# Kernel tuning notes

Hardware: AMD Instinct MI355X
Metric: run time of the kernel (lower is better)

Reference implementation:

```python
import jax, jax.numpy as jnp
import numpy as np

EMBD = 16
NUM_NODES = 100000
NUM_EDGES = 3200000
BN_EPS = 1e-5


def setup_inputs() -> dict:
    key = jax.random.key(0)
    ks = jax.random.split(key, 12)
    x = jax.random.normal(ks[0], (NUM_NODES, EMBD), dtype=jnp.float32)
    edge_index = jax.random.randint(ks[1], (2, NUM_EDGES), 0, NUM_NODES, dtype=jnp.int64)
    edge_attr = jax.random.normal(ks[2], (NUM_EDGES, EMBD), dtype=jnp.float32)
    s = 1.0 / np.sqrt(EMBD)  # torch Linear default init scale
    W0 = jax.random.uniform(ks[3], (EMBD, EMBD), jnp.float32, -s, s)
    b0 = jax.random.uniform(ks[4], (EMBD,), jnp.float32, -s, s)
    W1 = jax.random.uniform(ks[5], (EMBD, EMBD), jnp.float32, -s, s)
    b1 = jax.random.uniform(ks[6], (EMBD,), jnp.float32, -s, s)
    W2 = jax.random.uniform(ks[7], (EMBD, EMBD), jnp.float32, -s, s)
    b2 = jax.random.uniform(ks[8], (EMBD,), jnp.float32, -s, s)
    gamma = jnp.ones((EMBD,), jnp.float32)
    beta = jnp.zeros((EMBD,), jnp.float32)
    return {"x": x, "edge_index": edge_index, "edge_attr": edge_attr,
            "W0": W0, "b0": b0, "W1": W1, "b1": b1, "W2": W2, "b2": b2,
            "gamma": gamma, "beta": beta}


def reference(x, edge_index, edge_attr, W0, b0, W1, b1, W2, b2, gamma, beta):
    # Gather source/dest node features per edge: (num_edges, embd)
    h_src = x[edge_index[0]]
    h_dest = x[edge_index[1]]
    # Three small linears (torch Linear: y = x @ W.T + b), summed
    e = (edge_attr @ W0.T + b0) + (h_src @ W1.T + b1) + (h_dest @ W2.T + b2)
    # BatchNorm1d in training mode: biased batch statistics over edge dim
    mean = jnp.mean(e, axis=0)
    var = jnp.var(e, axis=0)  # biased, matches torch normalization
    e = (e - mean) * jax.lax.rsqrt(var + BN_EPS) * gamma + beta
    # ReLU + residual
    return edge_attr + jax.nn.relu(e)
```

## Files before the change

kernel.cpp:

```cpp
#include <hip/hip_runtime.h>
#include <math.h>

#define NN 100000
#define NE 3200000

constexpr int BLK = 256;
constexpr int GRID_EDGE = 2048;

typedef float f4 __attribute__((ext_vector_type(4)));
typedef _Float16 h4 __attribute__((ext_vector_type(4)));
typedef _Float16 h8 __attribute__((ext_vector_type(8)));


__device__ __forceinline__ void matvec16_acc(const float* __restrict__ sW,
                                             const float v[16], float acc[16]) {
#pragma unroll
  for (int j = 0; j < 16; ++j) {
    float a = acc[j];
#pragma unroll
    for (int q = 0; q < 4; ++q) {
      float4 w = ((const float4*)(sW + j * 16))[q];
      a = fmaf(v[q * 4 + 0], w.x, a);
      a = fmaf(v[q * 4 + 1], w.y, a);
      a = fmaf(v[q * 4 + 2], w.z, a);
      a = fmaf(v[q * 4 + 3], w.w, a);
    }
    acc[j] = a;
  }
}

__device__ __forceinline__ void load_row16(const float* __restrict__ base,
                                           size_t row, float v[16]) {
  const f4* r = (const f4*)(base + row * 16);
#pragma unroll
  for (int q = 0; q < 4; ++q) {
    f4 t = r[q];
    v[q * 4 + 0] = t[0]; v[q * 4 + 1] = t[1];
    v[q * 4 + 2] = t[2]; v[q * 4 + 3] = t[3];
  }
}

__device__ __forceinline__ void load_row16_nt(const float* __restrict__ base,
                                              size_t row, float v[16]) {
  const f4* r = (const f4*)(base + row * 16);
#pragma unroll
  for (int q = 0; q < 4; ++q) {
    f4 t = __builtin_nontemporal_load(r + q);
    v[q * 4 + 0] = t[0]; v[q * 4 + 1] = t[1];
    v[q * 4 + 2] = t[2]; v[q * 4 + 3] = t[3];
  }
}

__device__ __forceinline__ h8 pack_h8(const float* v) {
  h8 o;
#pragma unroll
  for (int i = 0; i < 8; ++i) o[i] = (_Float16)v[i];
  return o;
}

__global__ __launch_bounds__(BLK)
void node_proj(const float* __restrict__ x, const float* __restrict__ W1,
               const float* __restrict__ W2, h8* __restrict__ p1h,
               h8* __restrict__ p2h) {
  __shared__ __align__(16) float sW1[256];
  __shared__ __align__(16) float sW2[256];
  for (int i = threadIdx.x; i < 256; i += BLK) { sW1[i] = W1[i]; sW2[i] = W2[i]; }
  __syncthreads();
  int n = blockIdx.x * BLK + threadIdx.x;
  if (n >= NN) return;
  float xv[16];
  load_row16(x, (size_t)n, xv);
  float y1[16], y2[16];
#pragma unroll
  for (int j = 0; j < 16; ++j) { y1[j] = 0.f; y2[j] = 0.f; }
  matvec16_acc(sW1, xv, y1);
  matvec16_acc(sW2, xv, y2);
  p1h[(size_t)n * 2 + 0] = pack_h8(y1);
  p1h[(size_t)n * 2 + 1] = pack_h8(y1 + 8);
  p2h[(size_t)n * 2 + 0] = pack_h8(y2);
  p2h[(size_t)n * 2 + 1] = pack_h8(y2 + 8);
}

template <bool TABS, bool EH>
__global__ __launch_bounds__(BLK)
void edge_pass1(const float* __restrict__ ea, const int* __restrict__ ei,
                const float* __restrict__ xO, const h8* __restrict__ p1h,
                const h8* __restrict__ p2h, const float* __restrict__ W0g,
                const float* __restrict__ W1g, const float* __restrict__ W2g,
                float* __restrict__ stats, _Float16* __restrict__ eh,
                float* __restrict__ out) {
  __shared__ __align__(16) float sW0[256];
  __shared__ __align__(16) float sW1[256];
  __shared__ __align__(16) float sW2[256];
  __shared__ float red[4][32];
  for (int i = threadIdx.x; i < 256; i += BLK) {
    sW0[i] = W0g[i];
    if (!TABS) { sW1[i] = W1g[i]; sW2[i] = W2g[i]; }
  }
  __syncthreads();

  float sum[16], ssq[16];
#pragma unroll
  for (int j = 0; j < 16; ++j) { sum[j] = 0.f; ssq[j] = 0.f; }

  const int total = gridDim.x * BLK;
  for (int e = blockIdx.x * BLK + threadIdx.x; e < NE; e += total) {
    int s = __builtin_nontemporal_load(ei + e);
    int d = __builtin_nontemporal_load(ei + NE + e);
    float eav[16];
    load_row16_nt(ea, (size_t)e, eav);
    float ev[16];
    if (TABS) {
      h8 a0 = p1h[(size_t)s * 2 + 0];
      h8 a1 = p1h[(size_t)s * 2 + 1];
      h8 b0 = p2h[(size_t)d * 2 + 0];
      h8 b1 = p2h[(size_t)d * 2 + 1];
#pragma unroll
      for (int j = 0; j < 8; ++j) {
        ev[j]     = (float)a0[j] + (float)b0[j];
        ev[8 + j] = (float)a1[j] + (float)b1[j];
      }
      matvec16_acc(sW0, eav, ev);
    } else {
      float xs[16], xd[16];
      load_row16(xO, (size_t)s, xs);
      load_row16(xO, (size_t)d, xd);
#pragma unroll
      for (int j = 0; j < 16; ++j) ev[j] = 0.f;
      matvec16_acc(sW0, eav, ev);
      matvec16_acc(sW1, xs, ev);
      matvec16_acc(sW2, xd, ev);
    }
#pragma unroll
    for (int j = 0; j < 16; ++j) {
      sum[j] += ev[j];
      ssq[j] = fmaf(ev[j], ev[j], ssq[j]);
    }
    if (EH) {
      h8* ep = (h8*)(eh + (size_t)e * 16);
      __builtin_nontemporal_store(pack_h8(ev), ep);
      __builtin_nontemporal_store(pack_h8(ev + 8), ep + 1);
    } else {
      f4* orow = (f4*)(out + (size_t)e * 16);
#pragma unroll
      for (int q = 0; q < 4; ++q) {
        f4 o;
        o[0] = ev[q * 4 + 0]; o[1] = ev[q * 4 + 1];
        o[2] = ev[q * 4 + 2]; o[3] = ev[q * 4 + 3];
        __builtin_nontemporal_store(o, orow + q);
      }
    }
  }

#pragma unroll
  for (int off = 32; off > 0; off >>= 1) {
#pragma unroll
    for (int j = 0; j < 16; ++j) {
      sum[j] += __shfl_down(sum[j], off);
      ssq[j] += __shfl_down(ssq[j], off);
    }
  }
  int wid = threadIdx.x >> 6;
  int lane = threadIdx.x & 63;
  if (lane == 0) {
#pragma unroll
    for (int j = 0; j < 16; ++j) {
      red[wid][j] = sum[j];
      red[wid][16 + j] = ssq[j];
    }
  }
  __syncthreads();
  if (threadIdx.x < 32) {
    float v = red[0][threadIdx.x] + red[1][threadIdx.x] +
              red[2][threadIdx.x] + red[3][threadIdx.x];
    atomicAdd(stats + threadIdx.x, v);
  }
}

__global__ void finalize_kernel(const float* __restrict__ stats,
                                const float* __restrict__ gamma,
                                const float* __restrict__ beta,
                                float* __restrict__ ss) {
  int j = threadIdx.x;
  if (j < 16) {
    const float inv_n = 1.0f / (float)NE;
    float mean = stats[j] * inv_n;
    float var = fmaf(-mean, mean, stats[16 + j] * inv_n);
    float sc = gamma[j] / sqrtf(var + 1e-5f);
    ss[j] = sc;
    ss[16 + j] = fmaf(-mean, sc, beta[j]);
  }
}

template <bool EH>
__global__ __launch_bounds__(BLK)
void edge_pass2(const float* __restrict__ ea, const _Float16* __restrict__ eh,
                const float* __restrict__ ssg, float* __restrict__ out) {
  __shared__ float sSS[32];
  if (threadIdx.x < 32) sSS[threadIdx.x] = ssg[threadIdx.x];
  __syncthreads();
  const int totalv = NE * 4;
  const int stride = gridDim.x * BLK;
  int i0 = blockIdx.x * BLK + threadIdx.x;
  int c = (i0 & 3) * 4;
  float sc0 = sSS[c + 0], sc1 = sSS[c + 1], sc2 = sSS[c + 2], sc3 = sSS[c + 3];
  float sh0 = sSS[16 + c + 0], sh1 = sSS[16 + c + 1];
  float sh2 = sSS[16 + c + 2], sh3 = sSS[16 + c + 3];
  for (int i = i0; i < totalv; i += stride) {
    f4 av = __builtin_nontemporal_load((const f4*)ea + i);
    f4 evv;
    if (EH) {
      h4 hv = __builtin_nontemporal_load((const h4*)eh + i);
      evv[0] = (float)hv[0]; evv[1] = (float)hv[1];
      evv[2] = (float)hv[2]; evv[3] = (float)hv[3];
    } else {
      evv = __builtin_nontemporal_load((const f4*)out + i);
    }
    f4 o;
    o[0] = av[0] + fmaxf(0.f, fmaf(evv[0], sc0, sh0));
    o[1] = av[1] + fmaxf(0.f, fmaf(evv[1], sc1, sh1));
    o[2] = av[2] + fmaxf(0.f, fmaf(evv[2], sc2, sh2));
    o[3] = av[3] + fmaxf(0.f, fmaf(evv[3], sc3, sh3));
    __builtin_nontemporal_store(o, (f4*)out + i);
  }
}

extern "C" void kernel_launch(void* const* d_in, const int* in_sizes, int n_in,
                              void* d_out, int out_size, void* d_ws, size_t ws_size,
                              hipStream_t stream) {
  const float* x     = (const float*)d_in[0];
  const int*   ei    = (const int*)d_in[1];
  const float* ea    = (const float*)d_in[2];
  const float* W0    = (const float*)d_in[3];
  const float* W1    = (const float*)d_in[5];
  const float* W2    = (const float*)d_in[7];
  const float* gamma = (const float*)d_in[9];
  const float* beta  = (const float*)d_in[10];
  float* out = (float*)d_out;

  float* ws    = (float*)d_ws;
  float* stats = ws;
  float* ss    = ws + 32;
  h8* p1h = (h8*)((char*)d_ws + 1024);
  h8* p2h = p1h + (size_t)NN * 2;
  _Float16* eh = (_Float16*)(p2h + (size_t)NN * 2);

  size_t need_tabs = 1024 + (size_t)NN * 64;
  size_t need_eh   = need_tabs + (size_t)NE * 32;
  bool has_tabs = ws_size >= need_tabs;
  bool has_eh   = ws_size >= need_eh;

  hipMemsetAsync(stats, 0, 32 * sizeof(float), stream);

  if (has_tabs) {
    node_proj<<<(NN + BLK - 1) / BLK, BLK, 0, stream>>>(x, W1, W2, p1h, p2h);
    if (has_eh)
      edge_pass1<true, true><<<GRID_EDGE, BLK, 0, stream>>>(
          ea, ei, x, p1h, p2h, W0, W1, W2, stats, eh, out);
    else
      edge_pass1<true, false><<<GRID_EDGE, BLK, 0, stream>>>(
          ea, ei, x, p1h, p2h, W0, W1, W2, stats, eh, out);
  } else {
    edge_pass1<false, false><<<GRID_EDGE, BLK, 0, stream>>>(
        ea, ei, x, p1h, p2h, W0, W1, W2, stats, eh, out);
  }

  finalize_kernel<<<1, 64, 0, stream>>>(stats, gamma, beta, ss);

  if (has_eh)
    edge_pass2<true><<<GRID_EDGE, BLK, 0, stream>>>(ea, eh, ss, out);
  else
    edge_pass2<false><<<GRID_EDGE, BLK, 0, stream>>>(ea, eh, ss, out);
}
```

Measured before the change: 578.9 us.

## Fold stats zeroing and BN finalize into neighbor kernels; prefetch edge indices

Removes the memset and the separate finalize kernel. Stats are now zeroed inside node_proj, and each edge_pass2 block computes the scale and shift itself. edge_pass1 software-prefetches the next iteration's source and destination indices and moves the edge_attr load after the gather loads, so latency overlaps. It also adds occupancy hints to the launch bounds. The risks are higher register pressure from the prefetch and redundant finalize work in every pass2 block.

```diff
diff --git a/kernel.cpp b/kernel.cpp
--- a/kernel.cpp
+++ b/kernel.cpp
@@ -61,9 +61,10 @@
 __global__ __launch_bounds__(BLK)
 void node_proj(const float* __restrict__ x, const float* __restrict__ W1,
                const float* __restrict__ W2, h8* __restrict__ p1h,
-               h8* __restrict__ p2h) {
+               h8* __restrict__ p2h, float* __restrict__ stats) {
   __shared__ __align__(16) float sW1[256];
   __shared__ __align__(16) float sW2[256];
+  if (blockIdx.x == 0 && threadIdx.x < 32) stats[threadIdx.x] = 0.f;
   for (int i = threadIdx.x; i < 256; i += BLK) { sW1[i] = W1[i]; sW2[i] = W2[i]; }
   __syncthreads();
   int n = blockIdx.x * BLK + threadIdx.x;
@@ -82,7 +83,7 @@
 }
 
 template <bool TABS, bool EH>
-__global__ __launch_bounds__(BLK)
+__global__ __launch_bounds__(BLK, 4)
 void edge_pass1(const float* __restrict__ ea, const int* __restrict__ ei,
                 const float* __restrict__ xO, const h8* __restrict__ p1h,
                 const h8* __restrict__ p2h, const float* __restrict__ W0g,
@@ -104,17 +105,27 @@
   for (int j = 0; j < 16; ++j) { sum[j] = 0.f; ssq[j] = 0.f; }
 
   const int total = gridDim.x * BLK;
-  for (int e = blockIdx.x * BLK + threadIdx.x; e < NE; e += total) {
-    int s = __builtin_nontemporal_load(ei + e);
-    int d = __builtin_nontemporal_load(ei + NE + e);
+  int e = blockIdx.x * BLK + threadIdx.x;
+  int s = 0, d = 0;
+  if (e < NE) {
+    s = __builtin_nontemporal_load(ei + e);
+    d = __builtin_nontemporal_load(ei + NE + e);
+  }
+  for (; e < NE; e += total) {
+    int en = e + total;
+    int sn = 0, dn = 0;
+    if (en < NE) {
+      sn = __builtin_nontemporal_load(ei + en);
+      dn = __builtin_nontemporal_load(ei + NE + en);
+    }
     float eav[16];
-    load_row16_nt(ea, (size_t)e, eav);
     float ev[16];
     if (TABS) {
       h8 a0 = p1h[(size_t)s * 2 + 0];
       h8 a1 = p1h[(size_t)s * 2 + 1];
       h8 b0 = p2h[(size_t)d * 2 + 0];
       h8 b1 = p2h[(size_t)d * 2 + 1];
+      load_row16_nt(ea, (size_t)e, eav);
 #pragma unroll
       for (int j = 0; j < 8; ++j) {
         ev[j]     = (float)a0[j] + (float)b0[j];
@@ -125,6 +136,7 @@
       float xs[16], xd[16];
       load_row16(xO, (size_t)s, xs);
       load_row16(xO, (size_t)d, xd);
+      load_row16_nt(ea, (size_t)e, eav);
 #pragma unroll
       for (int j = 0; j < 16; ++j) ev[j] = 0.f;
       matvec16_acc(sW0, eav, ev);
@@ -150,6 +162,7 @@
         __builtin_nontemporal_store(o, orow + q);
       }
     }
+    s = sn; d = dn;
   }
 
 #pragma unroll
@@ -177,27 +190,21 @@
   }
 }
 
-__global__ void finalize_kernel(const float* __restrict__ stats,
-                                const float* __restrict__ gamma,
-                                const float* __restrict__ beta,
-                                float* __restrict__ ss) {
-  int j = threadIdx.x;
-  if (j < 16) {
+template <bool EH>
+__global__ __launch_bounds__(BLK, 8)
+void edge_pass2(const float* __restrict__ ea, const _Float16* __restrict__ eh,
+                const float* __restrict__ stats, const float* __restrict__ gamma,
+                const float* __restrict__ beta, float* __restrict__ out) {
+  __shared__ float sSS[32];
+  if (threadIdx.x < 16) {
+    int j = threadIdx.x;
     const float inv_n = 1.0f / (float)NE;
     float mean = stats[j] * inv_n;
     float var = fmaf(-mean, mean, stats[16 + j] * inv_n);
     float sc = gamma[j] / sqrtf(var + 1e-5f);
-    ss[j] = sc;
-    ss[16 + j] = fmaf(-mean, sc, beta[j]);
-  }
-}
-
-template <bool EH>
-__global__ __launch_bounds__(BLK)
-void edge_pass2(const float* __restrict__ ea, const _Float16* __restrict__ eh,
-                const float* __restrict__ ssg, float* __restrict__ out) {
-  __shared__ float sSS[32];
-  if (threadIdx.x < 32) sSS[threadIdx.x] = ssg[threadIdx.x];
+    sSS[j] = sc;
+    sSS[16 + j] = fmaf(-mean, sc, beta[j]);
+  }
   __syncthreads();
   const int totalv = NE * 4;
   const int stride = gridDim.x * BLK;
@@ -238,9 +245,7 @@
   const float* beta  = (const float*)d_in[10];
   float* out = (float*)d_out;
 
-  float* ws    = (float*)d_ws;
-  float* stats = ws;
-  float* ss    = ws + 32;
+  float* stats = (float*)d_ws;
   h8* p1h = (h8*)((char*)d_ws + 1024);
   h8* p2h = p1h + (size_t)NN * 2;
   _Float16* eh = (_Float16*)(p2h + (size_t)NN * 2);
@@ -250,10 +255,8 @@
   bool has_tabs = ws_size >= need_tabs;
   bool has_eh   = ws_size >= need_eh;
 
-  hipMemsetAsync(stats, 0, 32 * sizeof(float), stream);
-
   if (has_tabs) {
-    node_proj<<<(NN + BLK - 1) / BLK, BLK, 0, stream>>>(x, W1, W2, p1h, p2h);
+    node_proj<<<(NN + BLK - 1) / BLK, BLK, 0, stream>>>(x, W1, W2, p1h, p2h, stats);
     if (has_eh)
       edge_pass1<true, true><<<GRID_EDGE, BLK, 0, stream>>>(
           ea, ei, x, p1h, p2h, W0, W1, W2, stats, eh, out);
@@ -261,14 +264,13 @@
       edge_pass1<true, false><<<GRID_EDGE, BLK, 0, stream>>>(
           ea, ei, x, p1h, p2h, W0, W1, W2, stats, eh, out);
   } else {
+    hipMemsetAsync(stats, 0, 32 * sizeof(float), stream);
     edge_pass1<false, false><<<GRID_EDGE, BLK, 0, stream>>>(
         ea, ei, x, p1h, p2h, W0, W1, W2, stats, eh, out);
   }
 
-  finalize_kernel<<<1, 64, 0, stream>>>(stats, gamma, beta, ss);
-
   if (has_eh)
-    edge_pass2<true><<<GRID_EDGE, BLK, 0, stream>>>(ea, eh, ss, out);
+    edge_pass2<true><<<GRID_EDGE, BLK, 0, stream>>>(ea, eh, stats, gamma, beta, out);
   else
-    edge_pass2<false><<<GRID_EDGE, BLK, 0, stream>>>(ea, eh, ss, out);
-}
+    edge_pass2<false><<<GRID_EDGE, BLK, 0, stream>>>(ea, eh, stats, gamma, beta, out);
+}
```

Measured after the change: 1.185 ms. +104.7%, slower.
